# Kernel optimization log

Hardware: AMD Instinct MI355X
Metric: run time of the kernel (lower is better)

The kernel has to match this reference:

```python
import jax, jax.numpy as jnp
import numpy as np

NUM_SLOTS = 24
EPS = 1e-5

def setup_inputs() -> dict:
    key = jax.random.key(0)
    k1, k2 = jax.random.split(key)
    x = jax.random.normal(k1, (4, 32, 200, 2048), dtype=jnp.float32)
    time = jax.random.randint(k2, (4, 2048), 0, NUM_SLOTS, dtype=jnp.int64)
    return {"x": x, "time": time}

def reference(x, time):
    # x: [b, c, n, t]; time: [b, t] int slot ids in [0, NUM_SLOTS)
    b, c, n, t = x.shape
    time = time[..., -t:]
    idx = time.reshape(b * t)

    # [b*t, n, c] layout matching x.permute(2,0,3,1).reshape(n, b*t, c) contraction
    xf = jnp.transpose(x, (0, 3, 2, 1)).reshape(b * t, n * c)

    # True segment-sum replaces the one-hot matmul; column L1-normalize == divide by slot count
    counts = jax.ops.segment_sum(jnp.ones((b * t,), x.dtype), idx, num_segments=NUM_SLOTS)
    denom = jnp.maximum(counts, 1e-12)[:, None]  # F.normalize eps-clamped norm

    sum_x = jax.ops.segment_sum(xf, idx, num_segments=NUM_SLOTS)            # [S, n*c]
    sum_x2 = jax.ops.segment_sum(xf * xf, idx, num_segments=NUM_SLOTS)      # [S, n*c]

    mean_slot = (sum_x / denom).reshape(NUM_SLOTS, n, c).mean(axis=1)       # [S, c]
    m2_slot = (sum_x2 / denom).reshape(NUM_SLOTS, n, c).mean(axis=1)        # [S, c]
    var_slot = m2_slot - mean_slot ** 2                                     # [S, c]

    # Embedding gather back per (b, t), broadcast over n
    sm = jnp.transpose(mean_slot[time], (0, 2, 1))[:, :, None, :]           # [b, c, 1, t]
    sv = jnp.transpose(var_slot[time], (0, 2, 1))[:, :, None, :]            # [b, c, 1, t]

    return (x - sm) / jnp.sqrt(sv + EPS)
```

## Files before the change

### kernel.cpp

```cpp
#include <hip/hip_runtime.h>
#include <math.h>

#define Bb 4
#define Cc 32
#define Nn 200
#define Tt 2048
#define Ss 24
#define EPSf 1e-5f
#define ROWS 50
#define NCH 4

typedef float f4 __attribute__((ext_vector_type(4)));
typedef int i4 __attribute__((ext_vector_type(4)));
typedef unsigned int u2 __attribute__((ext_vector_type(2)));

__device__ __forceinline__ unsigned rne_bf16(float f) {
    unsigned u = __float_as_uint(f);
    return (u + 0x7FFFu + ((u >> 16) & 1u)) >> 16;
}
__device__ __forceinline__ unsigned pack2(float a, float b) {
    return rne_bf16(a) | (rne_bf16(b) << 16);
}
__device__ __forceinline__ float lo16(unsigned u) { return __uint_as_float(u << 16); }
__device__ __forceinline__ float hi16(unsigned u) { return __uint_as_float(u & 0xFFFF0000u); }


template <bool USE16>
__global__ __launch_bounds__(256) void k_partial(const float* __restrict__ x,
                                                 const int* __restrict__ timei,
                                                 unsigned short* __restrict__ xb16,
                                                 float2* __restrict__ part,
                                                 int* __restrict__ cntpart) {
    __shared__ float lsum[Ss], lsq[Ss];
    __shared__ int   lcnt[Ss];
    const int tid = threadIdx.x;
    const int bx  = blockIdx.x;
    const int b   = bx >> 7;
    const int c   = (bx >> 2) & 31;
    const int nc  = bx & 3;
    const bool do_hist = (c == 0 && nc == 0);

    if (tid < Ss) { lsum[tid] = 0.f; lsq[tid] = 0.f; lcnt[tid] = 0; }
    __syncthreads();

    const int t0 = tid * 4;
    const i4 sl0 = *(const i4*)(timei + b * Tt + t0);
    const i4 sl1 = *(const i4*)(timei + b * Tt + t0 + 1024);

    const size_t plane = ((size_t)(b * Cc + c) * Nn + (size_t)nc * ROWS) * Tt;
    const float* bp = x + plane + t0;
    unsigned short* wp = xb16 + plane + t0;

    float s0=0,s1=0,s2=0,s3=0,s4=0,s5=0,s6=0,s7=0;
    float q0=0,q1=0,q2=0,q3=0,q4=0,q5=0,q6=0,q7=0;

#pragma unroll 5
    for (int r = 0; r < ROWS; ++r) {
        f4 v0, v1;
        if constexpr (USE16) {
            v0 = __builtin_nontemporal_load((const f4*)(bp + (size_t)r * Tt));
            v1 = __builtin_nontemporal_load((const f4*)(bp + (size_t)r * Tt + 1024));
            u2 w0, w1;
            w0[0] = pack2(v0[0], v0[1]); w0[1] = pack2(v0[2], v0[3]);
            w1[0] = pack2(v1[0], v1[1]); w1[1] = pack2(v1[2], v1[3]);
            *(u2*)(wp + (size_t)r * Tt)        = w0;
            *(u2*)(wp + (size_t)r * Tt + 1024) = w1;
        } else {
            v0 = *(const f4*)(bp + (size_t)r * Tt);
            v1 = *(const f4*)(bp + (size_t)r * Tt + 1024);
        }
        s0 += v0[0]; q0 += v0[0]*v0[0];
        s1 += v0[1]; q1 += v0[1]*v0[1];
        s2 += v0[2]; q2 += v0[2]*v0[2];
        s3 += v0[3]; q3 += v0[3]*v0[3];
        s4 += v1[0]; q4 += v1[0]*v1[0];
        s5 += v1[1]; q5 += v1[1]*v1[1];
        s6 += v1[2]; q6 += v1[2]*v1[2];
        s7 += v1[3]; q7 += v1[3]*v1[3];
    }

    atomicAdd(&lsum[sl0[0]], s0); atomicAdd(&lsq[sl0[0]], q0);
    atomicAdd(&lsum[sl0[1]], s1); atomicAdd(&lsq[sl0[1]], q1);
    atomicAdd(&lsum[sl0[2]], s2); atomicAdd(&lsq[sl0[2]], q2);
    atomicAdd(&lsum[sl0[3]], s3); atomicAdd(&lsq[sl0[3]], q3);
    atomicAdd(&lsum[sl1[0]], s4); atomicAdd(&lsq[sl1[0]], q4);
    atomicAdd(&lsum[sl1[1]], s5); atomicAdd(&lsq[sl1[1]], q5);
    atomicAdd(&lsum[sl1[2]], s6); atomicAdd(&lsq[sl1[2]], q6);
    atomicAdd(&lsum[sl1[3]], s7); atomicAdd(&lsq[sl1[3]], q7);
    if (do_hist) {
        atomicAdd(&lcnt[sl0[0]], 1); atomicAdd(&lcnt[sl0[1]], 1);
        atomicAdd(&lcnt[sl0[2]], 1); atomicAdd(&lcnt[sl0[3]], 1);
        atomicAdd(&lcnt[sl1[0]], 1); atomicAdd(&lcnt[sl1[1]], 1);
        atomicAdd(&lcnt[sl1[2]], 1); atomicAdd(&lcnt[sl1[3]], 1);
    }
    __syncthreads();

    if (tid < Ss) {
        part[(c * Ss + tid) * 16 + (b * NCH + nc)] = make_float2(lsum[tid], lsq[tid]);
        if (do_hist) cntpart[b * Ss + tid] = lcnt[tid];
    }
}

template <bool USE16>
__global__ __launch_bounds__(256) void k_norm(const float* __restrict__ x,
                                              const unsigned short* __restrict__ xb16,
                                              const int* __restrict__ timei,
                                              const float2* __restrict__ part,
                                              const int* __restrict__ cntpart,
                                              float* __restrict__ out) {
    __shared__ float lsum[Ss], lsq[Ss];
    __shared__ float s_mr[Ss], s_r[Ss];
    const int tid = threadIdx.x;
    const int bx  = blockIdx.x;
    const int b   = bx >> 7;
    const int c   = (bx >> 2) & 31;
    const int nc  = bx & 3;

    if (tid < Ss) { lsum[tid] = 0.f; lsq[tid] = 0.f; }
    __syncthreads();
    if (tid < 192) {
        const int s = tid >> 3, j = tid & 7;
        float2 p0 = part[(c * Ss + s) * 16 + 2 * j];
        float2 p1 = part[(c * Ss + s) * 16 + 2 * j + 1];
        atomicAdd(&lsum[s], p0.x + p1.x);
        atomicAdd(&lsq[s],  p0.y + p1.y);
    }
    __syncthreads();
    if (tid < Ss) {
        float cnt = (float)(cntpart[tid] + cntpart[Ss + tid] +
                            cntpart[2 * Ss + tid] + cntpart[3 * Ss + tid]);
        float denom = fmaxf(cnt, 1e-12f) * (float)Nn;
        float m  = lsum[tid] / denom;
        float m2 = lsq[tid]  / denom;
        float rr = 1.0f / sqrtf(m2 - m * m + EPSf);
        s_r[tid]  = rr;
        s_mr[tid] = m * rr;
    }
    __syncthreads();

    const int t0 = tid * 4;
    const i4 sl0 = *(const i4*)(timei + b * Tt + t0);
    const i4 sl1 = *(const i4*)(timei + b * Tt + t0 + 1024);
    const float rr0 = s_r[sl0[0]], mr0 = s_mr[sl0[0]];
    const float rr1 = s_r[sl0[1]], mr1 = s_mr[sl0[1]];
    const float rr2 = s_r[sl0[2]], mr2 = s_mr[sl0[2]];
    const float rr3 = s_r[sl0[3]], mr3 = s_mr[sl0[3]];
    const float rr4 = s_r[sl1[0]], mr4 = s_mr[sl1[0]];
    const float rr5 = s_r[sl1[1]], mr5 = s_mr[sl1[1]];
    const float rr6 = s_r[sl1[2]], mr6 = s_mr[sl1[2]];
    const float rr7 = s_r[sl1[3]], mr7 = s_mr[sl1[3]];

    const size_t plane = ((size_t)(b * Cc + c) * Nn + (size_t)nc * ROWS) * Tt;
    const unsigned short* rp = xb16 + plane + t0;
    const float* xp = x + plane + t0;
    float* op = out + plane + t0;

#pragma unroll 5
    for (int r = 0; r < ROWS; ++r) {
        f4 o0, o1;
        if constexpr (USE16) {
            u2 a0 = *(const u2*)(rp + (size_t)r * Tt);
            u2 a1 = *(const u2*)(rp + (size_t)r * Tt + 1024);
            o0[0] = fmaf(lo16(a0[0]), rr0, -mr0);
            o0[1] = fmaf(hi16(a0[0]), rr1, -mr1);
            o0[2] = fmaf(lo16(a0[1]), rr2, -mr2);
            o0[3] = fmaf(hi16(a0[1]), rr3, -mr3);
            o1[0] = fmaf(lo16(a1[0]), rr4, -mr4);
            o1[1] = fmaf(hi16(a1[0]), rr5, -mr5);
            o1[2] = fmaf(lo16(a1[1]), rr6, -mr6);
            o1[3] = fmaf(hi16(a1[1]), rr7, -mr7);
        } else {
            f4 v0 = *(const f4*)(xp + (size_t)r * Tt);
            f4 v1 = *(const f4*)(xp + (size_t)r * Tt + 1024);
            o0[0] = fmaf(v0[0], rr0, -mr0);
            o0[1] = fmaf(v0[1], rr1, -mr1);
            o0[2] = fmaf(v0[2], rr2, -mr2);
            o0[3] = fmaf(v0[3], rr3, -mr3);
            o1[0] = fmaf(v1[0], rr4, -mr4);
            o1[1] = fmaf(v1[1], rr5, -mr5);
            o1[2] = fmaf(v1[2], rr6, -mr6);
            o1[3] = fmaf(v1[3], rr7, -mr7);
        }
        __builtin_nontemporal_store(o0, (f4*)(op + (size_t)r * Tt));
        __builtin_nontemporal_store(o1, (f4*)(op + (size_t)r * Tt + 1024));
    }
}

extern "C" void kernel_launch(void* const* d_in, const int* in_sizes, int n_in,
                              void* d_out, int out_size, void* d_ws, size_t ws_size,
                              hipStream_t stream) {
    const float* x   = (const float*)d_in[0];
    const int* timei = (const int*)d_in[1];
    float* out = (float*)d_out;

    const size_t nb16 = (size_t)Bb * Cc * Nn * Tt * sizeof(unsigned short);
    const size_t npart = (size_t)Cc * Ss * 16 * sizeof(float2);
    const size_t ncnt  = (size_t)Bb * Ss * sizeof(int);

    if (ws_size >= nb16 + npart + ncnt) {
        unsigned short* xb16 = (unsigned short*)d_ws;
        float2* part = (float2*)((char*)d_ws + nb16);
        int* cnt = (int*)((char*)d_ws + nb16 + npart);
        k_partial<true><<<Bb * Cc * NCH, 256, 0, stream>>>(x, timei, xb16, part, cnt);
        k_norm<true><<<Bb * Cc * NCH, 256, 0, stream>>>(x, xb16, timei, part, cnt, out);
    } else {
        float2* part = (float2*)d_ws;
        int* cnt = (int*)((char*)d_ws + npart);
        k_partial<false><<<Bb * Cc * NCH, 256, 0, stream>>>(x, timei, nullptr, part, cnt);
        k_norm<false><<<Bb * Cc * NCH, 256, 0, stream>>>(x, nullptr, timei, part, cnt, out);
    }
}
```

Baseline: 111.5 us.

## Fuse stats and normalize into one cooperative kernel with register-held bf16 tiles

Replaces the two-kernel pipeline with a single cooperative kernel. Each thread keeps its 100 rows as packed bf16 in registers, a grid-wide sync separates the reduction from the normalize pass, and x is then used from registers instead of being spilled to a bf16 workspace and re-read. This removes the global bf16 write and read plus one launch. The costs are 256 blocks of 512 threads needing co-residency, very high register pressure from 200 unsigned values per thread (possible spills to scratch), and the grid-sync cost.

New measurement: 111.5 us. Within noise of the previous version (-0.0%).

```diff
diff --git a/kernel.cpp b/kernel.cpp
--- a/kernel.cpp
+++ b/kernel.cpp
@@ -1,5 +1,8 @@
 #include <hip/hip_runtime.h>
+#include <hip/hip_cooperative_groups.h>
 #include <math.h>
+
+namespace cg = cooperative_groups;
 
 #define Bb 4
 #define Cc 32
@@ -7,8 +10,6 @@
 #define Tt 2048
 #define Ss 24
 #define EPSf 1e-5f
-#define ROWS 50
-#define NCH 4
 
 typedef float f4 __attribute__((ext_vector_type(4)));
 typedef int i4 __attribute__((ext_vector_type(4)));
@@ -24,6 +25,102 @@
 __device__ __forceinline__ float lo16(unsigned u) { return __uint_as_float(u << 16); }
 __device__ __forceinline__ float hi16(unsigned u) { return __uint_as_float(u & 0xFFFF0000u); }
 
+__global__ __launch_bounds__(512, 2) void k_one(const float* __restrict__ x,
+                                                const int* __restrict__ timei,
+                                                float2* __restrict__ part,
+                                                int* __restrict__ cntpart,
+                                                float* __restrict__ out) {
+    __shared__ float lsum[Ss], lsq[Ss];
+    __shared__ int   lcnt[Ss];
+    __shared__ float s_r[Ss], s_mr[Ss];
+
+    const int tid = threadIdx.x;
+    const int bx  = blockIdx.x;
+    const int b   = bx >> 6;
+    const int c   = (bx >> 1) & 31;
+    const int nh  = bx & 1;
+    const bool do_hist = (c == 0 && nh == 0);
+
+    if (tid < Ss) { lsum[tid] = 0.f; lsq[tid] = 0.f; lcnt[tid] = 0; }
+    __syncthreads();
+
+    const int t0 = tid * 4;
+    const size_t plane = ((size_t)(b * Cc + c) * Nn + (size_t)nh * 100) * Tt;
+    const float* bp = x + plane + t0;
+
+    unsigned xb[200];
+    float s0 = 0.f, s1 = 0.f, s2 = 0.f, s3 = 0.f;
+    float q0 = 0.f, q1 = 0.f, q2 = 0.f, q3 = 0.f;
+
+#pragma unroll
+    for (int r = 0; r < 100; ++r) {
+        f4 v = *(const f4*)(bp + (size_t)r * Tt);
+        xb[2 * r]     = pack2(v[0], v[1]);
+        xb[2 * r + 1] = pack2(v[2], v[3]);
+        s0 += v[0]; q0 += v[0] * v[0];
+        s1 += v[1]; q1 += v[1] * v[1];
+        s2 += v[2]; q2 += v[2] * v[2];
+        s3 += v[3]; q3 += v[3] * v[3];
+    }
+
+    const i4 sl = *(const i4*)(timei + b * Tt + t0);
+    atomicAdd(&lsum[sl[0]], s0); atomicAdd(&lsq[sl[0]], q0);
+    atomicAdd(&lsum[sl[1]], s1); atomicAdd(&lsq[sl[1]], q1);
+    atomicAdd(&lsum[sl[2]], s2); atomicAdd(&lsq[sl[2]], q2);
+    atomicAdd(&lsum[sl[3]], s3); atomicAdd(&lsq[sl[3]], q3);
+    if (do_hist) {
+        atomicAdd(&lcnt[sl[0]], 1); atomicAdd(&lcnt[sl[1]], 1);
+        atomicAdd(&lcnt[sl[2]], 1); atomicAdd(&lcnt[sl[3]], 1);
+    }
+    __syncthreads();
+
+    if (tid < Ss) {
+        part[(c * Ss + tid) * 8 + (b * 2 + nh)] = make_float2(lsum[tid], lsq[tid]);
+        if (do_hist) cntpart[b * Ss + tid] = lcnt[tid];
+    }
+
+    cg::this_grid().sync();
+
+    if (tid < Ss) { lsum[tid] = 0.f; lsq[tid] = 0.f; }
+    __syncthreads();
+    if (tid < 192) {
+        const int s = tid >> 3, j = tid & 7;
+        float2 p = part[(c * Ss + s) * 8 + j];
+        atomicAdd(&lsum[s], p.x);
+        atomicAdd(&lsq[s],  p.y);
+    }
+    __syncthreads();
+    if (tid < Ss) {
+        float cnt = (float)(cntpart[tid] + cntpart[Ss + tid] +
+                            cntpart[2 * Ss + tid] + cntpart[3 * Ss + tid]);
+        float denom = fmaxf(cnt, 1e-12f) * (float)Nn;
+        float m  = lsum[tid] / denom;
+        float m2 = lsq[tid]  / denom;
+        float rr = 1.0f / sqrtf(m2 - m * m + EPSf);
+        s_r[tid]  = rr;
+        s_mr[tid] = m * rr;
+    }
+    __syncthreads();
+
+    const float rr0 = s_r[sl[0]], mr0 = s_mr[sl[0]];
+    const float rr1 = s_r[sl[1]], mr1 = s_mr[sl[1]];
+    const float rr2 = s_r[sl[2]], mr2 = s_mr[sl[2]];
+    const float rr3 = s_r[sl[3]], mr3 = s_mr[sl[3]];
+
+    float* op = out + plane + t0;
+#pragma unroll
+    for (int r = 0; r < 100; ++r) {
+        f4 o;
+        o[0] = fmaf(lo16(xb[2 * r]),     rr0, -mr0);
+        o[1] = fmaf(hi16(xb[2 * r]),     rr1, -mr1);
+        o[2] = fmaf(lo16(xb[2 * r + 1]), rr2, -mr2);
+        o[3] = fmaf(hi16(xb[2 * r + 1]), rr3, -mr3);
+        __builtin_nontemporal_store(o, (f4*)(op + (size_t)r * Tt));
+    }
+}
+
+#define ROWS 50
+#define NCH 4
 
 template <bool USE16>
 __global__ __launch_bounds__(256) void k_partial(const float* __restrict__ x,
@@ -193,7 +290,24 @@
     const int* timei = (const int*)d_in[1];
     float* out = (float*)d_out;
 
-    const size_t nb16 = (size_t)Bb * Cc * Nn * Tt * sizeof(unsigned short);
+    {
+        float2* part = (float2*)d_ws;
+        int* cnt = (int*)((char*)d_ws + (size_t)Cc * Ss * 8 * sizeof(float2));
+        int occ = 0;
+        hipError_t q = hipOccupancyMaxActiveBlocksPerMultiprocessor(&occ, k_one, 512, 0);
+        if (q == hipSuccess && occ >= 1) {
+            void* args[] = { (void*)&x, (void*)&timei, (void*)&part, (void*)&cnt, (void*)&out };
+            hipError_t rc = hipLaunchCooperativeKernel((const void*)k_one,
+                                                       dim3(Bb * Cc * 2), dim3(512),
+                                                       args, 0, stream);
+            if (rc == hipSuccess) return;
+            (void)hipGetLastError();
+        } else {
+            (void)hipGetLastError();
+        }
+    }
+
+    const size_t nb16  = (size_t)Bb * Cc * Nn * Tt * sizeof(unsigned short);
     const size_t npart = (size_t)Cc * Ss * 16 * sizeof(float2);
     const size_t ncnt  = (size_t)Bb * Ss * sizeof(int);
 
```

## Fuse stats and normalize kernels with grid barrier, keep bf16 rows in registers

Applied to the files above, without the earlier changes.

Merges the partial-sum and normalization kernels into one persistent kernel of 512 blocks that synchronises through a global atomic counter. Each thread keeps 40 of its 50 rows as packed bf16 in registers and re-reads only the last 10 rows from global memory. This removes the bf16 workspace write and read and the second kernel launch, cutting DRAM traffic. The costs are heavy register pressure (160 registers for the cached rows), which could cause spills, and a grid-wide spin barrier that only works if all 512 blocks are resident at once (launch bounds of 2 blocks per SM across 256 CUs).

Measured after the change: 163.4 us. 1.47x slower.

```diff
diff --git a/kernel.cpp b/kernel.cpp
--- a/kernel.cpp
+++ b/kernel.cpp
@@ -7,12 +7,11 @@
 #define Tt 2048
 #define Ss 24
 #define EPSf 1e-5f
-#define ROWS 50
-#define NCH 4
+#define GRID 512
+#define RKEEP 40
 
 typedef float f4 __attribute__((ext_vector_type(4)));
 typedef int i4 __attribute__((ext_vector_type(4)));
-typedef unsigned int u2 __attribute__((ext_vector_type(2)));
 
 __device__ __forceinline__ unsigned rne_bf16(float f) {
     unsigned u = __float_as_uint(f);
@@ -25,20 +24,24 @@
 __device__ __forceinline__ float hi16(unsigned u) { return __uint_as_float(u & 0xFFFF0000u); }
 
 
-template <bool USE16>
-__global__ __launch_bounds__(256) void k_partial(const float* __restrict__ x,
-                                                 const int* __restrict__ timei,
-                                                 unsigned short* __restrict__ xb16,
-                                                 float2* __restrict__ part,
-                                                 int* __restrict__ cntpart) {
+__global__ void k_zero(int* __restrict__ counter) { *counter = 0; }
+
+__global__ __launch_bounds__(256, 2) void k_fused(const float* __restrict__ x,
+                                                  const int* __restrict__ timei,
+                                                  float2* __restrict__ part,
+                                                  int* __restrict__ cntp,
+                                                  int* __restrict__ counter,
+                                                  float* __restrict__ out) {
     __shared__ float lsum[Ss], lsq[Ss];
     __shared__ int   lcnt[Ss];
+    __shared__ float s_r[Ss], s_mr[Ss];
+
     const int tid = threadIdx.x;
     const int bx  = blockIdx.x;
     const int b   = bx >> 7;
     const int c   = (bx >> 2) & 31;
-    const int nc  = bx & 3;
-    const bool do_hist = (c == 0 && nc == 0);
+    const int q   = bx & 3;
+    const bool do_hist = (c == 0 && q == 0);
 
     if (tid < Ss) { lsum[tid] = 0.f; lsq[tid] = 0.f; lcnt[tid] = 0; }
     __syncthreads();
@@ -47,27 +50,22 @@
     const i4 sl0 = *(const i4*)(timei + b * Tt + t0);
     const i4 sl1 = *(const i4*)(timei + b * Tt + t0 + 1024);
 
-    const size_t plane = ((size_t)(b * Cc + c) * Nn + (size_t)nc * ROWS) * Tt;
+    const size_t plane = ((size_t)(b * Cc + c) * Nn + (size_t)q * 50) * Tt;
     const float* bp = x + plane + t0;
-    unsigned short* wp = xb16 + plane + t0;
 
+    unsigned xb[RKEEP * 4];
     float s0=0,s1=0,s2=0,s3=0,s4=0,s5=0,s6=0,s7=0;
     float q0=0,q1=0,q2=0,q3=0,q4=0,q5=0,q6=0,q7=0;
 
-#pragma unroll 5
-    for (int r = 0; r < ROWS; ++r) {
-        f4 v0, v1;
-        if constexpr (USE16) {
-            v0 = __builtin_nontemporal_load((const f4*)(bp + (size_t)r * Tt));
-            v1 = __builtin_nontemporal_load((const f4*)(bp + (size_t)r * Tt + 1024));
-            u2 w0, w1;
-            w0[0] = pack2(v0[0], v0[1]); w0[1] = pack2(v0[2], v0[3]);
-            w1[0] = pack2(v1[0], v1[1]); w1[1] = pack2(v1[2], v1[3]);
-            *(u2*)(wp + (size_t)r * Tt)        = w0;
-            *(u2*)(wp + (size_t)r * Tt + 1024) = w1;
-        } else {
-            v0 = *(const f4*)(bp + (size_t)r * Tt);
-            v1 = *(const f4*)(bp + (size_t)r * Tt + 1024);
+#pragma unroll
+    for (int r = 0; r < 50; ++r) {
+        f4 v0 = *(const f4*)(bp + (size_t)r * Tt);
+        f4 v1 = *(const f4*)(bp + (size_t)r * Tt + 1024);
+        if (r < RKEEP) {
+            xb[r*4+0] = pack2(v0[0], v0[1]);
+            xb[r*4+1] = pack2(v0[2], v0[3]);
+            xb[r*4+2] = pack2(v1[0], v1[1]);
+            xb[r*4+3] = pack2(v1[2], v1[3]);
         }
         s0 += v0[0]; q0 += v0[0]*v0[0];
         s1 += v0[1]; q1 += v0[1]*v0[1];
@@ -96,25 +94,16 @@
     __syncthreads();
 
     if (tid < Ss) {
-        part[(c * Ss + tid) * 16 + (b * NCH + nc)] = make_float2(lsum[tid], lsq[tid]);
-        if (do_hist) cntpart[b * Ss + tid] = lcnt[tid];
+        part[(c * Ss + tid) * 16 + (b * 4 + q)] = make_float2(lsum[tid], lsq[tid]);
+        if (do_hist) cntp[b * Ss + tid] = lcnt[tid];
     }
-}
 
-template <bool USE16>
-__global__ __launch_bounds__(256) void k_norm(const float* __restrict__ x,
-                                              const unsigned short* __restrict__ xb16,
-                                              const int* __restrict__ timei,
-                                              const float2* __restrict__ part,
-                                              const int* __restrict__ cntpart,
-                                              float* __restrict__ out) {
-    __shared__ float lsum[Ss], lsq[Ss];
-    __shared__ float s_mr[Ss], s_r[Ss];
-    const int tid = threadIdx.x;
-    const int bx  = blockIdx.x;
-    const int b   = bx >> 7;
-    const int c   = (bx >> 2) & 31;
-    const int nc  = bx & 3;
+    if (tid == 0) {
+        __hip_atomic_fetch_add(counter, 1, __ATOMIC_ACQ_REL, __HIP_MEMORY_SCOPE_AGENT);
+        while (__hip_atomic_load(counter, __ATOMIC_ACQUIRE, __HIP_MEMORY_SCOPE_AGENT) < GRID)
+            __builtin_amdgcn_s_sleep(2);
+    }
+    __syncthreads();
 
     if (tid < Ss) { lsum[tid] = 0.f; lsq[tid] = 0.f; }
     __syncthreads();
@@ -127,9 +116,8 @@
     }
     __syncthreads();
     if (tid < Ss) {
-        float cnt = (float)(cntpart[tid] + cntpart[Ss + tid] +
-                            cntpart[2 * Ss + tid] + cntpart[3 * Ss + tid]);
-        float denom = fmaxf(cnt, 1e-12f) * (float)Nn;
+        int cnt = cntp[tid] + cntp[Ss + tid] + cntp[2 * Ss + tid] + cntp[3 * Ss + tid];
+        float denom = fmaxf((float)cnt, 1e-12f) * (float)Nn;
         float m  = lsum[tid] / denom;
         float m2 = lsq[tid]  / denom;
         float rr = 1.0f / sqrtf(m2 - m * m + EPSf);
@@ -138,9 +126,6 @@
     }
     __syncthreads();
 
-    const int t0 = tid * 4;
-    const i4 sl0 = *(const i4*)(timei + b * Tt + t0);
-    const i4 sl1 = *(const i4*)(timei + b * Tt + t0 + 1024);
     const float rr0 = s_r[sl0[0]], mr0 = s_mr[sl0[0]];
     const float rr1 = s_r[sl0[1]], mr1 = s_mr[sl0[1]];
     const float rr2 = s_r[sl0[2]], mr2 = s_mr[sl0[2]];
@@ -150,37 +135,34 @@
     const float rr6 = s_r[sl1[2]], mr6 = s_mr[sl1[2]];
     const float rr7 = s_r[sl1[3]], mr7 = s_mr[sl1[3]];
 
-    const size_t plane = ((size_t)(b * Cc + c) * Nn + (size_t)nc * ROWS) * Tt;
-    const unsigned short* rp = xb16 + plane + t0;
-    const float* xp = x + plane + t0;
     float* op = out + plane + t0;
-
-#pragma unroll 5
-    for (int r = 0; r < ROWS; ++r) {
+#pragma unroll
+    for (int r = 0; r < RKEEP; ++r) {
         f4 o0, o1;
-        if constexpr (USE16) {
-            u2 a0 = *(const u2*)(rp + (size_t)r * Tt);
-            u2 a1 = *(const u2*)(rp + (size_t)r * Tt + 1024);
-            o0[0] = fmaf(lo16(a0[0]), rr0, -mr0);
-            o0[1] = fmaf(hi16(a0[0]), rr1, -mr1);
-            o0[2] = fmaf(lo16(a0[1]), rr2, -mr2);
-            o0[3] = fmaf(hi16(a0[1]), rr3, -mr3);
-            o1[0] = fmaf(lo16(a1[0]), rr4, -mr4);
-            o1[1] = fmaf(hi16(a1[0]), rr5, -mr5);
-            o1[2] = fmaf(lo16(a1[1]), rr6, -mr6);
-            o1[3] = fmaf(hi16(a1[1]), rr7, -mr7);
-        } else {
-            f4 v0 = *(const f4*)(xp + (size_t)r * Tt);
-            f4 v1 = *(const f4*)(xp + (size_t)r * Tt + 1024);
-            o0[0] = fmaf(v0[0], rr0, -mr0);
-            o0[1] = fmaf(v0[1], rr1, -mr1);
-            o0[2] = fmaf(v0[2], rr2, -mr2);
-            o0[3] = fmaf(v0[3], rr3, -mr3);
-            o1[0] = fmaf(v1[0], rr4, -mr4);
-            o1[1] = fmaf(v1[1], rr5, -mr5);
-            o1[2] = fmaf(v1[2], rr6, -mr6);
-            o1[3] = fmaf(v1[3], rr7, -mr7);
-        }
+        o0[0] = fmaf(lo16(xb[r*4+0]), rr0, -mr0);
+        o0[1] = fmaf(hi16(xb[r*4+0]), rr1, -mr1);
+        o0[2] = fmaf(lo16(xb[r*4+1]), rr2, -mr2);
+        o0[3] = fmaf(hi16(xb[r*4+1]), rr3, -mr3);
+        o1[0] = fmaf(lo16(xb[r*4+2]), rr4, -mr4);
+        o1[1] = fmaf(hi16(xb[r*4+2]), rr5, -mr5);
+        o1[2] = fmaf(lo16(xb[r*4+3]), rr6, -mr6);
+        o1[3] = fmaf(hi16(xb[r*4+3]), rr7, -mr7);
+        __builtin_nontemporal_store(o0, (f4*)(op + (size_t)r * Tt));
+        __builtin_nontemporal_store(o1, (f4*)(op + (size_t)r * Tt + 1024));
+    }
+#pragma unroll
+    for (int r = RKEEP; r < 50; ++r) {
+        f4 v0 = *(const f4*)(bp + (size_t)r * Tt);
+        f4 v1 = *(const f4*)(bp + (size_t)r * Tt + 1024);
+        f4 o0, o1;
+        o0[0] = fmaf(v0[0], rr0, -mr0);
+        o0[1] = fmaf(v0[1], rr1, -mr1);
+        o0[2] = fmaf(v0[2], rr2, -mr2);
+        o0[3] = fmaf(v0[3], rr3, -mr3);
+        o1[0] = fmaf(v1[0], rr4, -mr4);
+        o1[1] = fmaf(v1[1], rr5, -mr5);
+        o1[2] = fmaf(v1[2], rr6, -mr6);
+        o1[3] = fmaf(v1[3], rr7, -mr7);
         __builtin_nontemporal_store(o0, (f4*)(op + (size_t)r * Tt));
         __builtin_nontemporal_store(o1, (f4*)(op + (size_t)r * Tt + 1024));
     }
@@ -193,20 +175,11 @@
     const int* timei = (const int*)d_in[1];
     float* out = (float*)d_out;
 
-    const size_t nb16 = (size_t)Bb * Cc * Nn * Tt * sizeof(unsigned short);
-    const size_t npart = (size_t)Cc * Ss * 16 * sizeof(float2);
-    const size_t ncnt  = (size_t)Bb * Ss * sizeof(int);
+    float2* part = (float2*)d_ws;
+    int* cntp    = (int*)((char*)d_ws + (size_t)Cc * Ss * 16 * sizeof(float2));
+    int* counter = (int*)((char*)d_ws + (size_t)Cc * Ss * 16 * sizeof(float2)
+                          + 128 * sizeof(int));
 
-    if (ws_size >= nb16 + npart + ncnt) {
-        unsigned short* xb16 = (unsigned short*)d_ws;
-        float2* part = (float2*)((char*)d_ws + nb16);
-        int* cnt = (int*)((char*)d_ws + nb16 + npart);
-        k_partial<true><<<Bb * Cc * NCH, 256, 0, stream>>>(x, timei, xb16, part, cnt);
-        k_norm<true><<<Bb * Cc * NCH, 256, 0, stream>>>(x, xb16, timei, part, cnt, out);
-    } else {
-        float2* part = (float2*)d_ws;
-        int* cnt = (int*)((char*)d_ws + npart);
-        k_partial<false><<<Bb * Cc * NCH, 256, 0, stream>>>(x, timei, nullptr, part, cnt);
-        k_norm<false><<<Bb * Cc * NCH, 256, 0, stream>>>(x, nullptr, timei, part, cnt, out);
-    }
+    k_zero<<<1, 1, 0, stream>>>(counter);
+    k_fused<<<GRID, 256, 0, stream>>>(x, timei, part, cntp, counter, out);
 }
```
